# Performance work log

Hardware: AMD Instinct MI355X
Metric: run time of the kernel (lower is better)

## Reference

```python
import jax, jax.numpy as jnp
import numpy as np
import math

N, C, CI, S, T, V = 64, 128, 32, 3, 64, 25  # batch, channels, inter_channels, num_subset, num_frame, num_node
EPS = 1e-5


def _make_pe(channel, joint_num, time_len, domain):
    # Faithful PositionalEncoding: pos over (t, j) raster, sin on even ch, cos on odd ch -> (1, C, T, V)
    if domain == 'spatial':
        pos = np.tile(np.arange(joint_num), time_len)
    else:
        pos = np.repeat(np.arange(time_len), joint_num)
    position = pos[:, None].astype(np.float64)
    div = np.exp(np.arange(0, channel, 2, dtype=np.float64) * (-math.log(10000.0) / channel))
    pe = np.zeros((time_len * joint_num, channel))
    pe[:, 0::2] = np.sin(position * div)
    pe[:, 1::2] = np.cos(position * div)
    pe = pe.reshape(time_len, joint_num, channel).transpose(2, 0, 1)[None]
    return jnp.asarray(pe, jnp.float32)


def _c1(x, w, b):
    # 1x1 Conv2d == channel GEMM: x (N,Cin,T,V), w (Cout,Cin)
    return jnp.einsum('nctv,oc->notv', x, w) + b[None, :, None, None]


def _bn(x, g, b, m, v):
    # BatchNorm2d in eval mode with running stats
    inv = g * jax.lax.rsqrt(v + EPS)
    return (x - m[None, :, None, None]) * inv[None, :, None, None] + b[None, :, None, None]


def _lrelu(x):
    return jax.nn.leaky_relu(x, 0.1)


def setup_inputs() -> dict:
    key = jax.random.key(0)
    ks = iter(jax.random.split(key, 48))

    def nrm(shape, s=0.05):
        return jax.random.normal(next(ks), shape, jnp.float32) * s

    inp = {}
    inp['x'] = jax.random.normal(next(ks), (N, C, T, V), jnp.float32)
    inp['pe_s'] = _make_pe(C, V, T, 'spatial')
    inp['pe_t'] = _make_pe(C, V, T, 'temporal')
    # spatial attention branch
    inp['w_in_s'] = nrm((2 * S * CI, C)); inp['b_in_s'] = nrm((2 * S * CI,))
    inp['alphas'] = jnp.ones((1, S, 1, 1), jnp.float32)
    inp['att0s'] = jnp.full((1, S, V, V), 1.0 / V, jnp.float32)
    inp['w_out_s'] = nrm((C, S * C)); inp['b_out_s'] = nrm((C,))
    inp['w_ff_s'] = nrm((C, C)); inp['b_ff_s'] = nrm((C,))
    # temporal attention branch
    inp['w_in_t'] = nrm((2 * S * CI, C)); inp['b_in_t'] = nrm((2 * S * CI,))
    inp['alphat'] = jnp.ones((1, S, 1, 1), jnp.float32)
    inp['att0t'] = jnp.tile(jnp.eye(T, dtype=jnp.float32)[None, None], (1, S, 1, 1))
    inp['w_out_t'] = nrm((C, S * C)); inp['b_out_t'] = nrm((C,))
    inp['w_ff_t'] = nrm((C, C)); inp['b_ff_t'] = nrm((C,))
    # BatchNorm (eval-mode) params for out_nets/ff_nets/out_nett/ff_nett
    for nm in ('out_s', 'ff_s', 'out_t', 'ff_t'):
        inp['g_' + nm] = 1.0 + nrm((C,))
        inp['be_' + nm] = nrm((C,))
        inp['m_' + nm] = nrm((C,), 0.1)
        inp['v_' + nm] = jax.random.uniform(next(ks), (C,), jnp.float32, 0.5, 1.5)
    return inp


def reference(x, pe_s, pe_t,
              w_in_s, b_in_s, alphas, att0s, w_out_s, b_out_s,
              w_ff_s, b_ff_s,
              w_in_t, b_in_t, alphat, att0t, w_out_t, b_out_t,
              w_ff_t, b_ff_t,
              g_out_s, be_out_s, m_out_s, v_out_s,
              g_ff_s, be_ff_s, m_ff_s, v_ff_s,
              g_out_t, be_out_t, m_out_t, v_out_t,
              g_ff_t, be_ff_t, m_ff_t, v_ff_t):
    n, c, t, v = x.shape
    s = alphas.shape[1]
    ci = w_in_s.shape[0] // (2 * s)
    # ---- spatial attention ----
    y = x + pe_s[:, :, :t]
    qk = _c1(y, w_in_s, b_in_s).reshape(n, 2 * s, ci, t, v)
    q, k = qk[:, :s], qk[:, s:]
    att_s = jnp.tanh(jnp.einsum('nsctu,nsctv->nsuv', q, k) / (ci * t)) * alphas + att0s
    y = jnp.einsum('nctu,nsuv->nsctv', x, att_s).reshape(n, s * c, t, v)
    y = _bn(_c1(y, w_out_s, b_out_s), g_out_s, be_out_s, m_out_s, v_out_s)
    y = _lrelu(x + y)  # downs1 == identity
    y2 = _bn(_c1(y, w_ff_s, b_ff_s), g_ff_s, be_ff_s, m_ff_s, v_ff_s)
    y = _lrelu(x + y2)  # downs2 == identity
    # ---- temporal attention ----
    z = y + pe_t[:, :, :t]
    qk = _c1(z, w_in_t, b_in_t).reshape(n, 2 * s, ci, t, v)
    q, k = qk[:, :s], qk[:, s:]
    att_t = jnp.tanh(jnp.einsum('nsctv,nscqv->nstq', q, k) / (ci * v)) * alphat + att0t
    z = jnp.einsum('nctv,nstq->nscqv', y, att_t).reshape(n, s * c, t, v)
    z = _bn(_c1(z, w_out_t, b_out_t), g_out_t, be_out_t, m_out_t, v_out_t)
    z = _lrelu(y + z)  # downt1 == identity
    z2 = _bn(_c1(z, w_ff_t, b_ff_t), g_ff_t, be_ff_t, m_ff_t, v_ff_t)
    z = _lrelu(y + z2)  # downt2 == identity
    return z
```

## Files before the change

kernel.cpp:

```cpp
#include <hip/hip_runtime.h>
#include <math.h>


#define EPS_ 1e-5f

typedef short bf16x8 __attribute__((ext_vector_type(8)));
typedef float f32x4 __attribute__((ext_vector_type(4)));

__device__ __forceinline__ unsigned short f2bf(float f) {
  unsigned u = __float_as_uint(f);
  unsigned r = u + 0x7fffu + ((u >> 16) & 1u);
  return (unsigned short)(r >> 16);
}
__device__ __forceinline__ float bf2f(unsigned short h) {
  return __uint_as_float((unsigned)h << 16);
}

struct SplitArgs {
  const float* src[6];
  unsigned short* dst[6];
  int K[6];
  int nfrag[6];
};
__global__ __launch_bounds__(64) void k_split_w(SplitArgs a) {
  const int mat = blockIdx.y;
  const int f = blockIdx.x;
  if (f >= a.nfrag[mat]) return;
  const int K = a.K[mat];
  const int ksteps = K >> 5;
  const int ot = f / ksteps, ks = f % ksteps;
  const int l = threadIdx.x;
  const float* sp = a.src[mat] + (size_t)(ot * 16 + (l & 15)) * K + ks * 32 + (l >> 4) * 8;
  float4 f0 = *(const float4*)sp;
  float4 f1 = *(const float4*)(sp + 4);
  float vals[8] = {f0.x, f0.y, f0.z, f0.w, f1.x, f1.y, f1.z, f1.w};
  unsigned short hi[8], lo[8];
#pragma unroll
  for (int j = 0; j < 8; ++j) {
    hi[j] = f2bf(vals[j]);
    lo[j] = f2bf(vals[j] - bf2f(hi[j]));
  }
  unsigned short* d = a.dst[mat] + (size_t)f * 1024 + l * 8;
  uint4 ph, pl;
  ph.x = hi[0] | ((unsigned)hi[1] << 16); ph.y = hi[2] | ((unsigned)hi[3] << 16);
  ph.z = hi[4] | ((unsigned)hi[5] << 16); ph.w = hi[6] | ((unsigned)hi[7] << 16);
  pl.x = lo[0] | ((unsigned)lo[1] << 16); pl.y = lo[2] | ((unsigned)lo[3] << 16);
  pl.z = lo[4] | ((unsigned)lo[5] << 16); pl.w = lo[6] | ((unsigned)lo[7] << 16);
  *(uint4*)d = ph;
  *(uint4*)(d + 512) = pl;
}

template <int KTOT, int OTOT, int EPI>
__global__ __launch_bounds__(256) void k_mfma_conv(
    const float* __restrict__ Yin, const float* __restrict__ pe,
    const unsigned short* __restrict__ WF, const float* __restrict__ bias,
    const float* __restrict__ g, const float* __restrict__ be,
    const float* __restrict__ bm, const float* __restrict__ bv,
    const float* __restrict__ res, float* __restrict__ out) {
  constexpr int KSTEPS = KTOT / 32;
  constexpr int NCHUNK = KTOT / 128;
  constexpr int OTILES = OTOT / 16;
  const size_t yin_ns = (size_t)KTOT * 1600;
  const size_t out_ns = (size_t)OTOT * 1600;

  __shared__ unsigned short Yhi[64][136];
  __shared__ unsigned short Ylo[64][136];
  __shared__ float ep0[OTOT], ep1[OTOT];

  const int tid = threadIdx.x;
  const int lane = tid & 63, wv = tid >> 6;
  const int n = blockIdx.y, p0 = blockIdx.x * 64;

  for (int i = tid; i < OTOT; i += 256) {
    if (EPI == 1) {
      float inv = g[i] * rsqrtf(bv[i] + EPS_);
      ep0[i] = inv;
      ep1[i] = be[i] + (bias[i] - bm[i]) * inv;
    } else {
      ep0[i] = bias[i];
    }
  }

  f32x4 acc[OTILES];
#pragma unroll
  for (int ot = 0; ot < OTILES; ++ot) acc[ot] = 0;

  const int pl = tid & 63, q = tid >> 6;
  for (int kc = 0; kc < NCHUNK; ++kc) {
    const float* src = Yin + (size_t)n * yin_ns + (size_t)(kc * 128 + q * 32) * 1600 + p0 + pl;
    const float* pes = pe ? pe + (size_t)(kc * 128 + q * 32) * 1600 + p0 + pl : (const float*)0;
#pragma unroll
    for (int r = 0; r < 8; ++r) {
      float v4[4];
#pragma unroll
      for (int i = 0; i < 4; ++i) {
        v4[i] = src[(size_t)(r * 4 + i) * 1600];
        if (pe) v4[i] += pes[(size_t)(r * 4 + i) * 1600];
      }
      unsigned short h[4], lw[4];
#pragma unroll
      for (int i = 0; i < 4; ++i) {
        h[i] = f2bf(v4[i]);
        lw[i] = f2bf(v4[i] - bf2f(h[i]));
      }
      uint2 ph, plo;
      ph.x = h[0] | ((unsigned)h[1] << 16);  ph.y = h[2] | ((unsigned)h[3] << 16);
      plo.x = lw[0] | ((unsigned)lw[1] << 16); plo.y = lw[2] | ((unsigned)lw[3] << 16);
      *(uint2*)&Yhi[pl][q * 32 + r * 4] = ph;
      *(uint2*)&Ylo[pl][q * 32 + r * 4] = plo;
    }
    __syncthreads();

    const int rowA = wv * 16 + (lane & 15);
    const int kg = (lane >> 4) * 8;
#pragma unroll
    for (int ks = 0; ks < 4; ++ks) {
      bf16x8 ahi = *(const bf16x8*)&Yhi[rowA][ks * 32 + kg];
      bf16x8 alo = *(const bf16x8*)&Ylo[rowA][ks * 32 + kg];
#pragma unroll
      for (int ot = 0; ot < OTILES; ++ot) {
        const unsigned short* wp =
            WF + (size_t)(ot * KSTEPS + kc * 4 + ks) * 1024 + (lane << 3);
        bf16x8 whi = *(const bf16x8*)wp;
        bf16x8 wlo = *(const bf16x8*)(wp + 512);
        acc[ot] = __builtin_amdgcn_mfma_f32_16x16x32_bf16(ahi, whi, acc[ot], 0, 0, 0);
        acc[ot] = __builtin_amdgcn_mfma_f32_16x16x32_bf16(alo, whi, acc[ot], 0, 0, 0);
        acc[ot] = __builtin_amdgcn_mfma_f32_16x16x32_bf16(ahi, wlo, acc[ot], 0, 0, 0);
      }
    }
    __syncthreads();
  }

  const int o_l = lane & 15;
  const int prow = p0 + wv * 16 + ((lane >> 4) << 2);
#pragma unroll
  for (int ot = 0; ot < OTILES; ++ot) {
    const int o = ot * 16 + o_l;
    f32x4 v = acc[ot];
    if (EPI == 1) {
      const float inv = ep0[o], beta = ep1[o];
      const f32x4 rv = *(const f32x4*)(res + (size_t)n * out_ns + (size_t)o * 1600 + prow);
#pragma unroll
      for (int j = 0; j < 4; ++j) {
        float val = v[j] * inv + beta + rv[j];
        v[j] = val > 0.f ? val : 0.1f * val;
      }
    } else {
      const float bo = ep0[o];
#pragma unroll
      for (int j = 0; j < 4; ++j) v[j] += bo;
    }
    *(f32x4*)(out + (size_t)n * out_ns + (size_t)o * 1600 + prow) = v;
  }
}

__global__ __launch_bounds__(256) void k_gram_s(
    const float* __restrict__ qk, const float* __restrict__ alphas,
    const float* __restrict__ att0, float* __restrict__ att) {
  const int s = blockIdx.x, n = blockIdx.y;
  const float* qb = qk + (size_t)(n * 6 + s) * 51200;
  const float* kb = qk + (size_t)(n * 6 + 3 + s) * 51200;
  __shared__ unsigned short Qhi[32][136], Qlo[32][136];
  __shared__ unsigned short Khi[32][136], Klo[32][136];
  const int tid = threadIdx.x;
  const int lane = tid & 63, wv = tid >> 6;
  const int mt = wv >> 1, nt = wv & 1;
  const int rowA = mt * 16 + (lane & 15);
  const int rowB = nt * 16 + (lane & 15);
  const int kg = (lane >> 4) * 8;
  f32x4 acc = 0;
  for (int kc = 0; kc < 16; ++kc) {
    for (int idx = tid; idx < 3200; idx += 256) {
      const int cp = idx / 1600, rem = idx - cp * 1600;
      const int t = rem / 25, u = rem - t * 25;
      const int kl = cp * 64 + t;
      float qv = qb[kc * 3200 + idx];
      float kv = kb[kc * 3200 + idx];
      unsigned short qh = f2bf(qv), kh = f2bf(kv);
      Qhi[u][kl] = qh; Qlo[u][kl] = f2bf(qv - bf2f(qh));
      Khi[u][kl] = kh; Klo[u][kl] = f2bf(kv - bf2f(kh));
    }
    __syncthreads();
#pragma unroll
    for (int ks = 0; ks < 4; ++ks) {
      bf16x8 qh = *(const bf16x8*)&Qhi[rowA][ks * 32 + kg];
      bf16x8 ql = *(const bf16x8*)&Qlo[rowA][ks * 32 + kg];
      bf16x8 kh = *(const bf16x8*)&Khi[rowB][ks * 32 + kg];
      bf16x8 kl = *(const bf16x8*)&Klo[rowB][ks * 32 + kg];
      acc = __builtin_amdgcn_mfma_f32_16x16x32_bf16(qh, kh, acc, 0, 0, 0);
      acc = __builtin_amdgcn_mfma_f32_16x16x32_bf16(ql, kh, acc, 0, 0, 0);
      acc = __builtin_amdgcn_mfma_f32_16x16x32_bf16(qh, kl, acc, 0, 0, 0);
    }
    __syncthreads();
  }
  const float al = alphas[s];
  float* ab = att + (size_t)(n * 3 + s) * 625;
  const int v = nt * 16 + (lane & 15);
  const int u0 = mt * 16 + ((lane >> 4) << 2);
  if (v < 25) {
#pragma unroll
    for (int j = 0; j < 4; ++j) {
      const int u = u0 + j;
      if (u < 25)
        ab[u * 25 + v] = tanhf(acc[j] * (1.0f / 2048.0f)) * al + att0[s * 625 + u * 25 + v];
    }
  }
}

__global__ __launch_bounds__(256) void k_gram_t(
    const float* __restrict__ qk, const float* __restrict__ alphat,
    const float* __restrict__ att0, float* __restrict__ att) {
  const int s = blockIdx.x, n = blockIdx.y;
  const float* qb = qk + (size_t)(n * 6 + s) * 51200;
  const float* kb = qk + (size_t)(n * 6 + 3 + s) * 51200;
  __shared__ unsigned short Qhi[64][136], Qlo[64][136];
  __shared__ unsigned short Khi[64][136], Klo[64][136];
  const int tid = threadIdx.x;
  const int lane = tid & 63, wv = tid >> 6;
  const int rowA = wv * 16 + (lane & 15);
  const int kg = (lane >> 4) * 8;
  for (int idx = tid; idx < 64 * 28; idx += 256) {
    const int t = idx / 28, r = idx - t * 28;
    const int col = (r / 7) * 32 + 25 + (r % 7);
    Qhi[t][col] = 0; Qlo[t][col] = 0; Khi[t][col] = 0; Klo[t][col] = 0;
  }
  f32x4 acc[4];
#pragma unroll
  for (int nt = 0; nt < 4; ++nt) acc[nt] = 0;
  for (int cc = 0; cc < 8; ++cc) {
    for (int idx = tid; idx < 6400; idx += 256) {
      const int cp = idx / 1600, rem = idx - cp * 1600;
      const int t = rem / 25, v = rem - t * 25;
      const int kl = cp * 32 + v;
      float qv = qb[cc * 6400 + idx];
      float kv = kb[cc * 6400 + idx];
      unsigned short qh = f2bf(qv), kh = f2bf(kv);
      Qhi[t][kl] = qh; Qlo[t][kl] = f2bf(qv - bf2f(qh));
      Khi[t][kl] = kh; Klo[t][kl] = f2bf(kv - bf2f(kh));
    }
    __syncthreads();
#pragma unroll
    for (int ks = 0; ks < 4; ++ks) {
      bf16x8 qh = *(const bf16x8*)&Qhi[rowA][ks * 32 + kg];
      bf16x8 ql = *(const bf16x8*)&Qlo[rowA][ks * 32 + kg];
#pragma unroll
      for (int nt = 0; nt < 4; ++nt) {
        const int rowB = nt * 16 + (lane & 15);
        bf16x8 kh = *(const bf16x8*)&Khi[rowB][ks * 32 + kg];
        bf16x8 kl = *(const bf16x8*)&Klo[rowB][ks * 32 + kg];
        acc[nt] = __builtin_amdgcn_mfma_f32_16x16x32_bf16(qh, kh, acc[nt], 0, 0, 0);
        acc[nt] = __builtin_amdgcn_mfma_f32_16x16x32_bf16(ql, kh, acc[nt], 0, 0, 0);
        acc[nt] = __builtin_amdgcn_mfma_f32_16x16x32_bf16(qh, kl, acc[nt], 0, 0, 0);
      }
    }
    __syncthreads();
  }
  const float al = alphat[s];
  float* ab = att + (size_t)(n * 3 + s) * 4096;
  const int t0 = wv * 16 + ((lane >> 4) << 2);
  const int qcol = lane & 15;
#pragma unroll
  for (int nt = 0; nt < 4; ++nt) {
#pragma unroll
    for (int j = 0; j < 4; ++j) {
      const int t = t0 + j, q = nt * 16 + qcol;
      ab[t * 64 + q] =
          tanhf(acc[nt][j] * (1.0f / 800.0f)) * al + att0[(size_t)s * 4096 + t * 64 + q];
    }
  }
}

__global__ __launch_bounds__(256) void k_apply_s(
    const float* __restrict__ x, const float* __restrict__ att,
    float* __restrict__ ya) {
  const int t = blockIdx.x, n = blockIdx.y;
  __shared__ float xs[128][25];
  __shared__ float al[1875];
  const float* xb = x + (size_t)n * 204800 + t * 25;
  for (int idx = threadIdx.x; idx < 3200; idx += 256)
    xs[idx / 25][idx % 25] = xb[(size_t)(idx / 25) * 1600 + idx % 25];
  for (int idx = threadIdx.x; idx < 1875; idx += 256)
    al[idx] = att[(size_t)n * 1875 + idx];
  __syncthreads();
  float* yb = ya + (size_t)n * 614400 + t * 25;
  for (int idx = threadIdx.x; idx < 9600; idx += 256) {
    const int s = idx / 3200, rem = idx - s * 3200;
    const int c = rem / 25, v = rem % 25;
    const float* ap = al + s * 625 + v;
    float a = 0.f;
#pragma unroll
    for (int u = 0; u < 25; ++u) a += xs[c][u] * ap[u * 25];
    yb[(size_t)(s * 128 + c) * 1600 + v] = a;
  }
}

__global__ __launch_bounds__(256) void k_apply_t(
    const float* __restrict__ y, const float* __restrict__ att,
    float* __restrict__ mid) {
  const int cg = blockIdx.x, n2 = blockIdx.y;
  __shared__ float ys[3200];
  const float* ybase = y + ((size_t)n2 * 128 + cg * 2) * 1600;
  for (int idx = threadIdx.x; idx < 3200; idx += 256) ys[idx] = ybase[idx];
  __syncthreads();
  const float* ab = att + (size_t)n2 * 3 * 4096;
  for (int item = threadIdx.x; item < 1200; item += 256) {
    const int s = item / 400, rem = item % 400, qg = rem / 25, v = rem % 25;
    const int q0 = qg * 4;
    const float* ap = ab + s * 4096 + q0;
    float acc[2][4] = {};
#pragma unroll 4
    for (int t = 0; t < 64; ++t) {
      float4 av = *(const float4*)(ap + t * 64);
      float y0 = ys[t * 25 + v];
      float y1 = ys[1600 + t * 25 + v];
      acc[0][0] += y0 * av.x; acc[0][1] += y0 * av.y; acc[0][2] += y0 * av.z; acc[0][3] += y0 * av.w;
      acc[1][0] += y1 * av.x; acc[1][1] += y1 * av.y; acc[1][2] += y1 * av.z; acc[1][3] += y1 * av.w;
    }
    float* mb = mid + (((size_t)n2 * 3 + s) * 128 + cg * 2) * 1600 + v;
#pragma unroll
    for (int ci = 0; ci < 2; ++ci)
#pragma unroll
      for (int qj = 0; qj < 4; ++qj)
        mb[(size_t)ci * 1600 + (q0 + qj) * 25] = acc[ci][qj];
  }
}

extern "C" void kernel_launch(void* const* d_in, const int* in_sizes, int n_in,
                              void* d_out, int out_size, void* d_ws, size_t ws_size,
                              hipStream_t stream) {
  const float* x       = (const float*)d_in[0];
  const float* pe_s    = (const float*)d_in[1];
  const float* pe_t    = (const float*)d_in[2];
  const float* w_in_s  = (const float*)d_in[3];
  const float* b_in_s  = (const float*)d_in[4];
  const float* alphas  = (const float*)d_in[5];
  const float* att0s   = (const float*)d_in[6];
  const float* w_out_s = (const float*)d_in[7];
  const float* b_out_s = (const float*)d_in[8];
  const float* w_ff_s  = (const float*)d_in[9];
  const float* b_ff_s  = (const float*)d_in[10];
  const float* w_in_t  = (const float*)d_in[11];
  const float* b_in_t  = (const float*)d_in[12];
  const float* alphat  = (const float*)d_in[13];
  const float* att0t   = (const float*)d_in[14];
  const float* w_out_t = (const float*)d_in[15];
  const float* b_out_t = (const float*)d_in[16];
  const float* w_ff_t  = (const float*)d_in[17];
  const float* b_ff_t  = (const float*)d_in[18];
  const float* g_out_s  = (const float*)d_in[19];
  const float* be_out_s = (const float*)d_in[20];
  const float* m_out_s  = (const float*)d_in[21];
  const float* v_out_s  = (const float*)d_in[22];
  const float* g_ff_s   = (const float*)d_in[23];
  const float* be_ff_s  = (const float*)d_in[24];
  const float* m_ff_s   = (const float*)d_in[25];
  const float* v_ff_s   = (const float*)d_in[26];
  const float* g_out_t  = (const float*)d_in[27];
  const float* be_out_t = (const float*)d_in[28];
  const float* m_out_t  = (const float*)d_in[29];
  const float* v_out_t  = (const float*)d_in[30];
  const float* g_ff_t   = (const float*)d_in[31];
  const float* be_ff_t  = (const float*)d_in[32];
  const float* m_ff_t   = (const float*)d_in[33];
  const float* v_ff_t   = (const float*)d_in[34];
  (void)in_sizes; (void)n_in; (void)out_size;

  float* ws = (float*)d_ws;
  float* OUT = (float*)d_out;
  const size_t NS = 204800;

  const bool full = ws_size >= (size_t)134938624;
  float* SCR;
  float* ATT;
  float* YB;
  unsigned short* WF;
  if (full) {
    SCR = ws; ATT = ws + 19660800; YB = ws + 20447232;
    WF = (unsigned short*)(ws + 33554432);
  } else {
    SCR = ws; ATT = ws + 4915200; YB = ws + 5701632;
    WF = (unsigned short*)(ws + 18808832);
  }

  SplitArgs sa;
  sa.src[0] = w_in_s;  sa.dst[0] = WF + 0;       sa.K[0] = 128; sa.nfrag[0] = 48;
  sa.src[1] = w_out_s; sa.dst[1] = WF + 49152;   sa.K[1] = 384; sa.nfrag[1] = 96;
  sa.src[2] = w_ff_s;  sa.dst[2] = WF + 147456;  sa.K[2] = 128; sa.nfrag[2] = 32;
  sa.src[3] = w_in_t;  sa.dst[3] = WF + 180224;  sa.K[3] = 128; sa.nfrag[3] = 48;
  sa.src[4] = w_out_t; sa.dst[4] = WF + 229376;  sa.K[4] = 384; sa.nfrag[4] = 96;
  sa.src[5] = w_ff_t;  sa.dst[5] = WF + 327680;  sa.K[5] = 128; sa.nfrag[5] = 32;
  k_split_w<<<dim3(96, 6), 64, 0, stream>>>(sa);

  dim3 blk(256);
  const float* nul = (const float*)0;

  if (full) {
    k_mfma_conv<128, 192, 0><<<dim3(25, 64), blk, 0, stream>>>(
        x, pe_s, WF + 0, b_in_s, nul, nul, nul, nul, nul, SCR);
    k_gram_s<<<dim3(3, 64), blk, 0, stream>>>(SCR, alphas, att0s, ATT);
    for (int h = 0; h < 2; ++h) {
      k_apply_s<<<dim3(64, 32), blk, 0, stream>>>(
          x + (size_t)h * 32 * NS, ATT + (size_t)h * 32 * 1875, SCR);
      k_mfma_conv<384, 128, 1><<<dim3(25, 32), blk, 0, stream>>>(
          SCR, nul, WF + 49152, b_out_s, g_out_s, be_out_s, m_out_s, v_out_s,
          x + (size_t)h * 32 * NS, OUT + (size_t)h * 32 * NS);
    }
    k_mfma_conv<128, 128, 1><<<dim3(25, 64), blk, 0, stream>>>(
        OUT, nul, WF + 147456, b_ff_s, g_ff_s, be_ff_s, m_ff_s, v_ff_s, x, YB);
    k_mfma_conv<128, 192, 0><<<dim3(25, 64), blk, 0, stream>>>(
        YB, pe_t, WF + 180224, b_in_t, nul, nul, nul, nul, nul, SCR);
    k_gram_t<<<dim3(3, 64), blk, 0, stream>>>(SCR, alphat, att0t, ATT);
    for (int h = 0; h < 2; ++h) {
      k_apply_t<<<dim3(64, 32), blk, 0, stream>>>(
          YB + (size_t)h * 32 * NS, ATT + (size_t)h * 32 * 12288, SCR);
      k_mfma_conv<384, 128, 1><<<dim3(25, 32), blk, 0, stream>>>(
          SCR, nul, WF + 229376, b_out_t, g_out_t, be_out_t, m_out_t, v_out_t,
          YB + (size_t)h * 32 * NS, OUT + (size_t)h * 32 * NS);
    }
    k_mfma_conv<128, 128, 1><<<dim3(25, 64), blk, 0, stream>>>(
        OUT, nul, WF + 327680, b_ff_t, g_ff_t, be_ff_t, m_ff_t, v_ff_t, YB, OUT);
  } else {
    for (int h = 0; h < 4; ++h) {
      k_mfma_conv<128, 192, 0><<<dim3(25, 16), blk, 0, stream>>>(
          x + (size_t)h * 16 * NS, pe_s, WF + 0, b_in_s, nul, nul, nul, nul, nul, SCR);
      k_gram_s<<<dim3(3, 16), blk, 0, stream>>>(SCR, alphas, att0s,
                                                ATT + (size_t)h * 16 * 1875);
    }
    for (int e = 0; e < 8; ++e) {
      k_apply_s<<<dim3(64, 8), blk, 0, stream>>>(
          x + (size_t)e * 8 * NS, ATT + (size_t)e * 8 * 1875, SCR);
      k_mfma_conv<384, 128, 1><<<dim3(25, 8), blk, 0, stream>>>(
          SCR, nul, WF + 49152, b_out_s, g_out_s, be_out_s, m_out_s, v_out_s,
          x + (size_t)e * 8 * NS, OUT + (size_t)e * 8 * NS);
    }
    k_mfma_conv<128, 128, 1><<<dim3(25, 64), blk, 0, stream>>>(
        OUT, nul, WF + 147456, b_ff_s, g_ff_s, be_ff_s, m_ff_s, v_ff_s, x, YB);
    for (int h = 0; h < 4; ++h) {
      k_mfma_conv<128, 192, 0><<<dim3(25, 16), blk, 0, stream>>>(
          YB + (size_t)h * 16 * NS, pe_t, WF + 180224, b_in_t, nul, nul, nul, nul, nul, SCR);
      k_gram_t<<<dim3(3, 16), blk, 0, stream>>>(SCR, alphat, att0t,
                                                ATT + (size_t)h * 16 * 12288);
    }
    for (int e = 0; e < 8; ++e) {
      k_apply_t<<<dim3(64, 8), blk, 0, stream>>>(
          YB + (size_t)e * 8 * NS, ATT + (size_t)e * 8 * 12288, SCR);
      k_mfma_conv<384, 128, 1><<<dim3(25, 8), blk, 0, stream>>>(
          SCR, nul, WF + 229376, b_out_t, g_out_t, be_out_t, m_out_t, v_out_t,
          YB + (size_t)e * 8 * NS, OUT + (size_t)e * 8 * NS);
    }
    k_mfma_conv<128, 128, 1><<<dim3(25, 64), blk, 0, stream>>>(
        OUT, nul, WF + 327680, b_ff_t, g_ff_t, be_ff_t, m_ff_t, v_ff_t, YB, OUT);
  }
}
```

Before: 1.036 ms.

## Replace LDS-staged conv GEMM with register-direct loads and per-wave multi-tile reuse

The 1x1 conv MFMA kernel no longer stages activations through LDS with block barriers. Each lane now loads its A fragment straight from global memory into registers, prefetching the next K step. The hi part of the bf16 split becomes a truncation, and the epilogue BN constants are computed inline. Output/out-proj convs use 128-thread blocks where each wave handles two 16-pixel tiles, so each weight fragment is used twice. This removes LDS traffic and syncs, but uses more registers and does strided, less coalesced global loads.

```diff
diff --git a/kernel.cpp b/kernel.cpp
--- a/kernel.cpp
+++ b/kernel.cpp
@@ -50,107 +50,117 @@
   *(uint4*)(d + 512) = pl;
 }
 
-template <int KTOT, int OTOT, int EPI>
-__global__ __launch_bounds__(256) void k_mfma_conv(
+template <int KTOT, int OTOT, int EPI, int PT, bool HASPE>
+__global__ __launch_bounds__(256 / PT) void k_conv_reg(
     const float* __restrict__ Yin, const float* __restrict__ pe,
     const unsigned short* __restrict__ WF, const float* __restrict__ bias,
     const float* __restrict__ g, const float* __restrict__ be,
     const float* __restrict__ bm, const float* __restrict__ bv,
     const float* __restrict__ res, float* __restrict__ out) {
   constexpr int KSTEPS = KTOT / 32;
-  constexpr int NCHUNK = KTOT / 128;
   constexpr int OTILES = OTOT / 16;
+  constexpr int WAVES = (256 / PT) / 64;
   const size_t yin_ns = (size_t)KTOT * 1600;
   const size_t out_ns = (size_t)OTOT * 1600;
-
-  __shared__ unsigned short Yhi[64][136];
-  __shared__ unsigned short Ylo[64][136];
-  __shared__ float ep0[OTOT], ep1[OTOT];
-
-  const int tid = threadIdx.x;
-  const int lane = tid & 63, wv = tid >> 6;
-  const int n = blockIdx.y, p0 = blockIdx.x * 64;
-
-  for (int i = tid; i < OTOT; i += 256) {
-    if (EPI == 1) {
-      float inv = g[i] * rsqrtf(bv[i] + EPS_);
-      ep0[i] = inv;
-      ep1[i] = be[i] + (bias[i] - bm[i]) * inv;
-    } else {
-      ep0[i] = bias[i];
-    }
-  }
-
-  f32x4 acc[OTILES];
-#pragma unroll
-  for (int ot = 0; ot < OTILES; ++ot) acc[ot] = 0;
-
-  const int pl = tid & 63, q = tid >> 6;
-  for (int kc = 0; kc < NCHUNK; ++kc) {
-    const float* src = Yin + (size_t)n * yin_ns + (size_t)(kc * 128 + q * 32) * 1600 + p0 + pl;
-    const float* pes = pe ? pe + (size_t)(kc * 128 + q * 32) * 1600 + p0 + pl : (const float*)0;
-#pragma unroll
-    for (int r = 0; r < 8; ++r) {
-      float v4[4];
+  const int tid = threadIdx.x, lane = tid & 63, wv = tid >> 6;
+  const int n = blockIdx.y;
+  const int p0 = (blockIdx.x * WAVES + wv) * (PT * 16);
+  const int krow = (lane >> 4) * 8;
+  const float* Yb = Yin + (size_t)n * yin_ns;
+
+  f32x4 acc[PT][OTILES];
+#pragma unroll
+  for (int pp = 0; pp < PT; ++pp)
+#pragma unroll
+    for (int ot = 0; ot < OTILES; ++ot) acc[pp][ot] = 0;
+
+  float af[PT][8];
+#pragma unroll
+  for (int j = 0; j < 8; ++j) {
+    const size_t ko = (size_t)(krow + j) * 1600;
+#pragma unroll
+    for (int pp = 0; pp < PT; ++pp) {
+      const int pc = p0 + pp * 16 + (lane & 15);
+      float v = Yb[ko + pc];
+      if (HASPE) v += pe[ko + pc];
+      af[pp][j] = v;
+    }
+  }
+
+  for (int ks = 0; ks < KSTEPS; ++ks) {
+    float an[PT][8];
+    if (ks + 1 < KSTEPS) {
+#pragma unroll
+      for (int j = 0; j < 8; ++j) {
+        const size_t ko = (size_t)((ks + 1) * 32 + krow + j) * 1600;
+#pragma unroll
+        for (int pp = 0; pp < PT; ++pp) {
+          const int pc = p0 + pp * 16 + (lane & 15);
+          float v = Yb[ko + pc];
+          if (HASPE) v += pe[ko + pc];
+          an[pp][j] = v;
+        }
+      }
+    }
+    bf16x8 ahi[PT], alo[PT];
+#pragma unroll
+    for (int pp = 0; pp < PT; ++pp) {
+      union { unsigned u[4]; bf16x8 v; } ch, cl;
 #pragma unroll
       for (int i = 0; i < 4; ++i) {
-        v4[i] = src[(size_t)(r * 4 + i) * 1600];
-        if (pe) v4[i] += pes[(size_t)(r * 4 + i) * 1600];
+        const float fa = af[pp][2 * i], fb = af[pp][2 * i + 1];
+        const unsigned ua = __float_as_uint(fa), ub = __float_as_uint(fb);
+        ch.u[i] = (ua >> 16) | (ub & 0xffff0000u);
+        const float ra = fa - __uint_as_float(ua & 0xffff0000u);
+        const float rb = fb - __uint_as_float(ub & 0xffff0000u);
+        cl.u[i] = (unsigned)f2bf(ra) | ((unsigned)f2bf(rb) << 16);
       }
-      unsigned short h[4], lw[4];
-#pragma unroll
-      for (int i = 0; i < 4; ++i) {
-        h[i] = f2bf(v4[i]);
-        lw[i] = f2bf(v4[i] - bf2f(h[i]));
+      ahi[pp] = ch.v; alo[pp] = cl.v;
+    }
+#pragma unroll
+    for (int ot = 0; ot < OTILES; ++ot) {
+      const unsigned short* wp = WF + (size_t)(ot * KSTEPS + ks) * 1024 + (lane << 3);
+      bf16x8 whi = *(const bf16x8*)wp;
+      bf16x8 wlo = *(const bf16x8*)(wp + 512);
+#pragma unroll
+      for (int pp = 0; pp < PT; ++pp) {
+        acc[pp][ot] = __builtin_amdgcn_mfma_f32_16x16x32_bf16(ahi[pp], whi, acc[pp][ot], 0, 0, 0);
+        acc[pp][ot] = __builtin_amdgcn_mfma_f32_16x16x32_bf16(alo[pp], whi, acc[pp][ot], 0, 0, 0);
+        acc[pp][ot] = __builtin_amdgcn_mfma_f32_16x16x32_bf16(ahi[pp], wlo, acc[pp][ot], 0, 0, 0);
       }
-      uint2 ph, plo;
-      ph.x = h[0] | ((unsigned)h[1] << 16);  ph.y = h[2] | ((unsigned)h[3] << 16);
-      plo.x = lw[0] | ((unsigned)lw[1] << 16); plo.y = lw[2] | ((unsigned)lw[3] << 16);
-      *(uint2*)&Yhi[pl][q * 32 + r * 4] = ph;
-      *(uint2*)&Ylo[pl][q * 32 + r * 4] = plo;
-    }
-    __syncthreads();
-
-    const int rowA = wv * 16 + (lane & 15);
-    const int kg = (lane >> 4) * 8;
-#pragma unroll
-    for (int ks = 0; ks < 4; ++ks) {
-      bf16x8 ahi = *(const bf16x8*)&Yhi[rowA][ks * 32 + kg];
-      bf16x8 alo = *(const bf16x8*)&Ylo[rowA][ks * 32 + kg];
-#pragma unroll
-      for (int ot = 0; ot < OTILES; ++ot) {
-        const unsigned short* wp =
-            WF + (size_t)(ot * KSTEPS + kc * 4 + ks) * 1024 + (lane << 3);
-        bf16x8 whi = *(const bf16x8*)wp;
-        bf16x8 wlo = *(const bf16x8*)(wp + 512);
-        acc[ot] = __builtin_amdgcn_mfma_f32_16x16x32_bf16(ahi, whi, acc[ot], 0, 0, 0);
-        acc[ot] = __builtin_amdgcn_mfma_f32_16x16x32_bf16(alo, whi, acc[ot], 0, 0, 0);
-        acc[ot] = __builtin_amdgcn_mfma_f32_16x16x32_bf16(ahi, wlo, acc[ot], 0, 0, 0);
+    }
+    if (ks + 1 < KSTEPS) {
+#pragma unroll
+      for (int pp = 0; pp < PT; ++pp)
+#pragma unroll
+        for (int j = 0; j < 8; ++j) af[pp][j] = an[pp][j];
+    }
+  }
+
+  const int o_l = lane & 15;
+#pragma unroll
+  for (int pp = 0; pp < PT; ++pp) {
+    const int prow = p0 + pp * 16 + ((lane >> 4) << 2);
+#pragma unroll
+    for (int ot = 0; ot < OTILES; ++ot) {
+      const int o = ot * 16 + o_l;
+      f32x4 v = acc[pp][ot];
+      if (EPI == 1) {
+        const float inv = g[o] * rsqrtf(bv[o] + EPS_);
+        const float beta = be[o] + (bias[o] - bm[o]) * inv;
+        const f32x4 rv = *(const f32x4*)(res + (size_t)n * out_ns + (size_t)o * 1600 + prow);
+#pragma unroll
+        for (int j = 0; j < 4; ++j) {
+          float val = v[j] * inv + beta + rv[j];
+          v[j] = val > 0.f ? val : 0.1f * val;
+        }
+      } else {
+        const float bo = bias[o];
+#pragma unroll
+        for (int j = 0; j < 4; ++j) v[j] += bo;
       }
-    }
-    __syncthreads();
-  }
-
-  const int o_l = lane & 15;
-  const int prow = p0 + wv * 16 + ((lane >> 4) << 2);
-#pragma unroll
-  for (int ot = 0; ot < OTILES; ++ot) {
-    const int o = ot * 16 + o_l;
-    f32x4 v = acc[ot];
-    if (EPI == 1) {
-      const float inv = ep0[o], beta = ep1[o];
-      const f32x4 rv = *(const f32x4*)(res + (size_t)n * out_ns + (size_t)o * 1600 + prow);
-#pragma unroll
-      for (int j = 0; j < 4; ++j) {
-        float val = v[j] * inv + beta + rv[j];
-        v[j] = val > 0.f ? val : 0.1f * val;
-      }
-    } else {
-      const float bo = ep0[o];
-#pragma unroll
-      for (int j = 0; j < 4; ++j) v[j] += bo;
-    }
-    *(f32x4*)(out + (size_t)n * out_ns + (size_t)o * 1600 + prow) = v;
+      *(f32x4*)(out + (size_t)n * out_ns + (size_t)o * 1600 + prow) = v;
+    }
   }
 }
 
@@ -391,37 +401,37 @@
   sa.src[5] = w_ff_t;  sa.dst[5] = WF + 327680;  sa.K[5] = 128; sa.nfrag[5] = 32;
   k_split_w<<<dim3(96, 6), 64, 0, stream>>>(sa);
 
-  dim3 blk(256);
+  dim3 blk(256), blk2(128);
   const float* nul = (const float*)0;
 
   if (full) {
-    k_mfma_conv<128, 192, 0><<<dim3(25, 64), blk, 0, stream>>>(
+    k_conv_reg<128, 192, 0, 1, true><<<dim3(25, 64), blk, 0, stream>>>(
         x, pe_s, WF + 0, b_in_s, nul, nul, nul, nul, nul, SCR);
     k_gram_s<<<dim3(3, 64), blk, 0, stream>>>(SCR, alphas, att0s, ATT);
     for (int h = 0; h < 2; ++h) {
       k_apply_s<<<dim3(64, 32), blk, 0, stream>>>(
           x + (size_t)h * 32 * NS, ATT + (size_t)h * 32 * 1875, SCR);
-      k_mfma_conv<384, 128, 1><<<dim3(25, 32), blk, 0, stream>>>(
+      k_conv_reg<384, 128, 1, 2, false><<<dim3(25, 32), blk2, 0, stream>>>(
           SCR, nul, WF + 49152, b_out_s, g_out_s, be_out_s, m_out_s, v_out_s,
           x + (size_t)h * 32 * NS, OUT + (size_t)h * 32 * NS);
     }
-    k_mfma_conv<128, 128, 1><<<dim3(25, 64), blk, 0, stream>>>(
+    k_conv_reg<128, 128, 1, 2, false><<<dim3(25, 64), blk2, 0, stream>>>(
         OUT, nul, WF + 147456, b_ff_s, g_ff_s, be_ff_s, m_ff_s, v_ff_s, x, YB);
-    k_mfma_conv<128, 192, 0><<<dim3(25, 64), blk, 0, stream>>>(
+    k_conv_reg<128, 192, 0, 1, true><<<dim3(25, 64), blk, 0, stream>>>(
         YB, pe_t, WF + 180224, b_in_t, nul, nul, nul, nul, nul, SCR);
     k_gram_t<<<dim3(3, 64), blk, 0, stream>>>(SCR, alphat, att0t, ATT);
     for (int h = 0; h < 2; ++h) {
       k_apply_t<<<dim3(64, 32), blk, 0, stream>>>(
           YB + (size_t)h * 32 * NS, ATT + (size_t)h * 32 * 12288, SCR);
-      k_mfma_conv<384, 128, 1><<<dim3(25, 32), blk, 0, stream>>>(
+      k_conv_reg<384, 128, 1, 2, false><<<dim3(25, 32), blk2, 0, stream>>>(
           SCR, nul, WF + 229376, b_out_t, g_out_t, be_out_t, m_out_t, v_out_t,
           YB + (size_t)h * 32 * NS, OUT + (size_t)h * 32 * NS);
     }
-    k_mfma_conv<128, 128, 1><<<dim3(25, 64), blk, 0, stream>>>(
+    k_conv_reg<128, 128, 1, 2, false><<<dim3(25, 64), blk2, 0, stream>>>(
         OUT, nul, WF + 327680, b_ff_t, g_ff_t, be_ff_t, m_ff_t, v_ff_t, YB, OUT);
   } else {
     for (int h = 0; h < 4; ++h) {
-      k_mfma_conv<128, 192, 0><<<dim3(25, 16), blk, 0, stream>>>(
+      k_conv_reg<128, 192, 0, 1, true><<<dim3(25, 16), blk, 0, stream>>>(
           x + (size_t)h * 16 * NS, pe_s, WF + 0, b_in_s, nul, nul, nul, nul, nul, SCR);
       k_gram_s<<<dim3(3, 16), blk, 0, stream>>>(SCR, alphas, att0s,
                                                 ATT + (size_t)h * 16 * 1875);
@@ -429,14 +439,14 @@
     for (int e = 0; e < 8; ++e) {
       k_apply_s<<<dim3(64, 8), blk, 0, stream>>>(
           x + (size_t)e * 8 * NS, ATT + (size_t)e * 8 * 1875, SCR);
-      k_mfma_conv<384, 128, 1><<<dim3(25, 8), blk, 0, stream>>>(
+      k_conv_reg<384, 128, 1, 2, false><<<dim3(25, 8), blk2, 0, stream>>>(
           SCR, nul, WF + 49152, b_out_s, g_out_s, be_out_s, m_out_s, v_out_s,
           x + (size_t)e * 8 * NS, OUT + (size_t)e * 8 * NS);
     }
-    k_mfma_conv<128, 128, 1><<<dim3(25, 64), blk, 0, stream>>>(
+    k_conv_reg<128, 128, 1, 2, false><<<dim3(25, 64), blk2, 0, stream>>>(
         OUT, nul, WF + 147456, b_ff_s, g_ff_s, be_ff_s, m_ff_s, v_ff_s, x, YB);
     for (int h = 0; h < 4; ++h) {
-      k_mfma_conv<128, 192, 0><<<dim3(25, 16), blk, 0, stream>>>(
+      k_conv_reg<128, 192, 0, 1, true><<<dim3(25, 16), blk, 0, stream>>>(
           YB + (size_t)h * 16 * NS, pe_t, WF + 180224, b_in_t, nul, nul, nul, nul, nul, SCR);
       k_gram_t<<<dim3(3, 16), blk, 0, stream>>>(SCR, alphat, att0t,
                                                 ATT + (size_t)h * 16 * 12288);
@@ -444,11 +454,11 @@
     for (int e = 0; e < 8; ++e) {
       k_apply_t<<<dim3(64, 8), blk, 0, stream>>>(
           YB + (size_t)e * 8 * NS, ATT + (size_t)e * 8 * 12288, SCR);
-      k_mfma_conv<384, 128, 1><<<dim3(25, 8), blk, 0, stream>>>(
+      k_conv_reg<384, 128, 1, 2, false><<<dim3(25, 8), blk2, 0, stream>>>(
           SCR, nul, WF + 229376, b_out_t, g_out_t, be_out_t, m_out_t, v_out_t,
           YB + (size_t)e * 8 * NS, OUT + (size_t)e * 8 * NS);
     }
-    k_mfma_conv<128, 128, 1><<<dim3(25, 64), blk, 0, stream>>>(
+    k_conv_reg<128, 128, 1, 2, false><<<dim3(25, 64), blk2, 0, stream>>>(
         OUT, nul, WF + 327680, b_ff_t, g_ff_t, be_ff_t, m_ff_t, v_ff_t, YB, OUT);
   }
 }
```

Result: faster. 895.6 us (-13.6%).
